# Optimization experiments

Measured on AMD Instinct MI355X. Metric: run time of the kernel, lower is better.

Reference implementation:

```python
import jax, jax.numpy as jnp
import numpy as np

B, N, C = 4, 2048, 768
H = 12
D = C // H  # 64
HID = 4 * C  # 3072
EPS = 1e-5


def layer_norm(x, g, b):
    mu = jnp.mean(x, axis=-1, keepdims=True)
    var = jnp.mean(jnp.square(x - mu), axis=-1, keepdims=True)
    return (x - mu) * jax.lax.rsqrt(var + EPS) * g + b


def setup_inputs() -> dict:
    key = jax.random.key(0)
    ks = jax.random.split(key, 12)
    s = lambda fan_in: 1.0 / np.sqrt(fan_in)
    return {
        "x": jax.random.normal(ks[0], (B, N, C), jnp.float32),
        "ln1_g": jnp.ones((C,), jnp.float32),
        "ln1_b": jnp.zeros((C,), jnp.float32),
        "qkv_w": jax.random.normal(ks[1], (3 * C, C), jnp.float32) * s(C),
        "proj_w": jax.random.normal(ks[2], (C, C), jnp.float32) * s(C),
        "proj_b": jnp.zeros((C,), jnp.float32),
        "ln2_g": jnp.ones((C,), jnp.float32),
        "ln2_b": jnp.zeros((C,), jnp.float32),
        "fc1_w": jax.random.normal(ks[3], (HID, C), jnp.float32) * s(C),
        "fc1_b": jnp.zeros((HID,), jnp.float32),
        "fc2_w": jax.random.normal(ks[4], (C, HID), jnp.float32) * s(HID),
        "fc2_b": jnp.zeros((C,), jnp.float32),
    }


def reference(x, ln1_g, ln1_b, qkv_w, proj_w, proj_b, ln2_g, ln2_b, fc1_w, fc1_b, fc2_w, fc2_b):
    # ---- attention branch ----
    h = layer_norm(x, ln1_g, ln1_b)
    qkv = jnp.einsum('bnc,fc->bnf', h, qkv_w)            # [B,N,3C]
    qkv = qkv.reshape(B, N, 3, H, D)
    q, k, v = jnp.moveaxis(qkv, 2, 0)                     # each [B,N,H,D]
    q = jnp.transpose(q, (0, 2, 1, 3)) * (D ** -0.5)      # [B,H,N,D]
    k = jnp.transpose(k, (0, 2, 1, 3))
    v = jnp.transpose(v, (0, 2, 1, 3))
    attn = jax.nn.softmax(jnp.einsum('bhnd,bhmd->bhnm', q, k), axis=-1)
    o = jnp.einsum('bhnm,bhmd->bhnd', attn, v)            # [B,H,N,D]
    o = jnp.transpose(o, (0, 2, 1, 3)).reshape(B, N, C)
    o = jnp.einsum('bnc,oc->bno', o, proj_w) + proj_b
    x = x + o
    # ---- MLP branch ----
    h = layer_norm(x, ln2_g, ln2_b)
    h = jnp.einsum('bnc,hc->bnh', h, fc1_w) + fc1_b
    h = jax.nn.gelu(h, approximate=False)
    h = jnp.einsum('bnh,ch->bnc', h, fc2_w) + fc2_b
    return x + h
```

## Files before the change

kernel.cpp:

```cpp
#include <hip/hip_runtime.h>
#include <math.h>

typedef __bf16 bf16;
typedef __bf16 bf16x4 __attribute__((ext_vector_type(4)));
typedef __bf16 bf16x8 __attribute__((ext_vector_type(8)));
typedef float  f32x4  __attribute__((ext_vector_type(4)));

#define B_   4
#define N_   2048
#define C_   768
#define H_   12
#define T_   8192
#define HID_ 3072

typedef const __attribute__((address_space(1))) unsigned int* as1_u32;
typedef __attribute__((address_space(3))) unsigned int* as3_u32;
__device__ __forceinline__ void gl_lds16(const void* g, void* l) {
    __builtin_amdgcn_global_load_lds((as1_u32)g, (as3_u32)l, 16, 0, 0);
}

__global__ __launch_bounds__(256)
void ln_kernel(const float* __restrict__ inp, const float* __restrict__ g,
               const float* __restrict__ bsh, bf16* __restrict__ out)
{
    int wave = threadIdx.x >> 6, lane = threadIdx.x & 63;
    long long row = (long long)blockIdx.x * 4 + wave;
    const float* p = inp + row * C_;
    float v[12];
    #pragma unroll
    for (int i = 0; i < 12; i++) v[i] = p[i * 64 + lane];
    float s = 0.f, s2 = 0.f;
    #pragma unroll
    for (int i = 0; i < 12; i++) { s += v[i]; s2 += v[i] * v[i]; }
    #pragma unroll
    for (int m = 1; m < 64; m <<= 1) {
        s  += __shfl_xor(s,  m, 64);
        s2 += __shfl_xor(s2, m, 64);
    }
    float mu  = s  * (1.f / C_);
    float var = s2 * (1.f / C_) - mu * mu;
    float rs  = rsqrtf(var + 1e-5f);
    bf16* o = out + row * C_;
    #pragma unroll
    for (int i = 0; i < 12; i++) {
        int c = i * 64 + lane;
        o[c] = (bf16)(((v[i] - mu) * rs) * g[c] + bsh[c]);
    }
}

template<int MODE>
__global__ __launch_bounds__(256)
void gemm_bt(const bf16* __restrict__ A, const float* __restrict__ Bw,
             int M, int N, int K,
             const float* __restrict__ bias,
             void* out, bf16* out2)
{
    __shared__ bf16 At[2][128 * 32];
    __shared__ bf16 Bt[2][128 * 32];
    int tid  = threadIdx.x;
    int lane = tid & 63, wave = tid >> 6;
    int quad = lane >> 4, l15 = lane & 15;
    int bm = blockIdx.x, bn = blockIdx.y;
    int wm = wave >> 1, wn = wave & 1;
    int swz = (l15 >> 1) & 3;

    f32x4 acc[4][4];
    f32x4 zero = {0.f, 0.f, 0.f, 0.f};
    #pragma unroll
    for (int mt = 0; mt < 4; mt++)
        #pragma unroll
        for (int nt = 0; nt < 4; nt++) acc[mt][nt] = zero;

    int arow = tid >> 2;
    int aq   = (tid & 3) ^ ((arow >> 1) & 3);
    const bf16*  ag0 = A  + (size_t)(bm * 128 + arow) * K + aq * 8;
    const float* bg0 = Bw + (size_t)(bn * 128 + arow) * K + aq * 8;

    gl_lds16(ag0,                    &At[0][tid * 8]);
    gl_lds16(ag0 + (size_t)64 * K,   &At[0][2048 + tid * 8]);
    {
        f32x4 b0a = *(const f32x4*)(bg0);
        f32x4 b0b = *(const f32x4*)(bg0 + 4);
        f32x4 b1a = *(const f32x4*)(bg0 + (size_t)64 * K);
        f32x4 b1b = *(const f32x4*)(bg0 + (size_t)64 * K + 4);
        bf16x8 b0, b1;
        #pragma unroll
        for (int j = 0; j < 4; j++) {
            b0[j] = (bf16)b0a[j]; b0[4 + j] = (bf16)b0b[j];
            b1[j] = (bf16)b1a[j]; b1[4 + j] = (bf16)b1b[j];
        }
        *(bf16x8*)(&Bt[0][tid * 8])        = b0;
        *(bf16x8*)(&Bt[0][2048 + tid * 8]) = b1;
    }
    __syncthreads();

    int nk = K >> 5;
    f32x4 pba, pbb, pca, pcb;
    for (int kt = 0; kt < nk; kt++) {
        int cur = kt & 1, nxt = cur ^ 1;
        if (kt + 1 < nk) {
            const bf16*  ag = ag0 + (size_t)(kt + 1) * 32;
            const float* bg = bg0 + (size_t)(kt + 1) * 32;
            gl_lds16(ag,                  &At[nxt][tid * 8]);
            gl_lds16(ag + (size_t)64 * K, &At[nxt][2048 + tid * 8]);
            pba = *(const f32x4*)(bg);
            pbb = *(const f32x4*)(bg + 4);
            pca = *(const f32x4*)(bg + (size_t)64 * K);
            pcb = *(const f32x4*)(bg + (size_t)64 * K + 4);
        }

        bf16x8 af[4], bfr[4];
        #pragma unroll
        for (int mt = 0; mt < 4; mt++)
            af[mt] = *(const bf16x8*)(&At[cur][wm * 2048 + (mt * 16 + l15) * 32 + ((quad ^ swz) << 3)]);
        #pragma unroll
        for (int nt = 0; nt < 4; nt++)
            bfr[nt] = *(const bf16x8*)(&Bt[cur][wn * 2048 + (nt * 16 + l15) * 32 + ((quad ^ swz) << 3)]);
        #pragma unroll
        for (int mt = 0; mt < 4; mt++)
            #pragma unroll
            for (int nt = 0; nt < 4; nt++)
                acc[mt][nt] = __builtin_amdgcn_mfma_f32_16x16x32_bf16(
                    af[mt], bfr[nt], acc[mt][nt], 0, 0, 0);

        if (kt + 1 < nk) {
            bf16x8 b0, b1;
            #pragma unroll
            for (int j = 0; j < 4; j++) {
                b0[j] = (bf16)pba[j]; b0[4 + j] = (bf16)pbb[j];
                b1[j] = (bf16)pca[j]; b1[4 + j] = (bf16)pcb[j];
            }
            *(bf16x8*)(&Bt[nxt][tid * 8])        = b0;
            *(bf16x8*)(&Bt[nxt][2048 + tid * 8]) = b1;
        }
        __syncthreads();
    }

    if (MODE == 3) {
        if (bn < 12) {
            #pragma unroll
            for (int nt = 0; nt < 4; nt++) {
                int col = bn * 128 + wn * 64 + nt * 16 + l15;
                #pragma unroll
                for (int mt = 0; mt < 4; mt++)
                    #pragma unroll
                    for (int r = 0; r < 4; r++) {
                        int row = bm * 128 + wm * 64 + mt * 16 + quad * 4 + r;
                        ((bf16*)out)[(size_t)row * 1536 + col] = (bf16)acc[mt][nt][r];
                    }
            }
        } else {
            int b = bm >> 4;
            #pragma unroll
            for (int nt = 0; nt < 4; nt++) {
                int vcol = bn * 128 - 1536 + wn * 64 + nt * 16 + l15;
                int h = vcol >> 6, d = vcol & 63;
                size_t rowbase = ((size_t)(b * H_ + h) * 64 + d) * N_;
                #pragma unroll
                for (int mt = 0; mt < 4; mt++) {
                    int n0 = (bm & 15) * 128 + wm * 64 + mt * 16 + quad * 4;
                    bf16x4 pv;
                    #pragma unroll
                    for (int r = 0; r < 4; r++) pv[r] = (bf16)acc[mt][nt][r];
                    *(bf16x4*)(&out2[rowbase + n0]) = pv;
                }
            }
        }
    } else {
        #pragma unroll
        for (int nt = 0; nt < 4; nt++) {
            int col = bn * 128 + wn * 64 + nt * 16 + l15;
            float bv = bias[col];
            #pragma unroll
            for (int mt = 0; mt < 4; mt++) {
                #pragma unroll
                for (int r = 0; r < 4; r++) {
                    int row = bm * 128 + wm * 64 + mt * 16 + quad * 4 + r;
                    size_t idx = (size_t)row * N + col;
                    float v = acc[mt][nt][r] + bv;
                    float ge = 0.5f * v * (1.f + erff(v * 0.70710678118f));
                    ((bf16*)out)[idx] = (bf16)ge;
                }
            }
        }
    }
}

__global__ __launch_bounds__(256)
void gemm64(const bf16* __restrict__ A, const float* __restrict__ Bw,
            int K, const float* __restrict__ bias,
            const float* resid_f, float* out)
{
    __shared__ bf16 At[2][128 * 32];
    __shared__ bf16 Bt[2][64 * 32];
    int tid  = threadIdx.x;
    int lane = tid & 63, wave = tid >> 6;
    int quad = lane >> 4, l15 = lane & 15;
    int bm = blockIdx.x, bn = blockIdx.y;
    int wm = wave >> 1, wn = wave & 1;
    int swz = (l15 >> 1) & 3;

    f32x4 acc[4][2];
    f32x4 zero = {0.f, 0.f, 0.f, 0.f};
    #pragma unroll
    for (int mt = 0; mt < 4; mt++)
        #pragma unroll
        for (int nt = 0; nt < 2; nt++) acc[mt][nt] = zero;

    int arow = tid >> 2;
    int aq   = (tid & 3) ^ ((arow >> 1) & 3);
    const bf16*  ag0 = A  + (size_t)(bm * 128 + arow) * K + aq * 8;
    const float* bg0 = Bw + (size_t)(bn * 64  + arow) * K + aq * 8;

    gl_lds16(ag0,                  &At[0][tid * 8]);
    gl_lds16(ag0 + (size_t)64 * K, &At[0][2048 + tid * 8]);
    {
        f32x4 ba = *(const f32x4*)(bg0);
        f32x4 bb = *(const f32x4*)(bg0 + 4);
        bf16x8 b0;
        #pragma unroll
        for (int j = 0; j < 4; j++) { b0[j] = (bf16)ba[j]; b0[4 + j] = (bf16)bb[j]; }
        *(bf16x8*)(&Bt[0][tid * 8]) = b0;
    }
    __syncthreads();

    int nk = K >> 5;
    f32x4 pba, pbb;
    for (int kt = 0; kt < nk; kt++) {
        int cur = kt & 1, nxt = cur ^ 1;
        if (kt + 1 < nk) {
            const bf16*  ag = ag0 + (size_t)(kt + 1) * 32;
            const float* bg = bg0 + (size_t)(kt + 1) * 32;
            gl_lds16(ag,                  &At[nxt][tid * 8]);
            gl_lds16(ag + (size_t)64 * K, &At[nxt][2048 + tid * 8]);
            pba = *(const f32x4*)(bg);
            pbb = *(const f32x4*)(bg + 4);
        }

        bf16x8 af[4], bfr[2];
        #pragma unroll
        for (int mt = 0; mt < 4; mt++)
            af[mt] = *(const bf16x8*)(&At[cur][wm * 2048 + (mt * 16 + l15) * 32 + ((quad ^ swz) << 3)]);
        #pragma unroll
        for (int nt = 0; nt < 2; nt++)
            bfr[nt] = *(const bf16x8*)(&Bt[cur][(wn * 32 + nt * 16 + l15) * 32 + ((quad ^ swz) << 3)]);
        #pragma unroll
        for (int mt = 0; mt < 4; mt++)
            #pragma unroll
            for (int nt = 0; nt < 2; nt++)
                acc[mt][nt] = __builtin_amdgcn_mfma_f32_16x16x32_bf16(
                    af[mt], bfr[nt], acc[mt][nt], 0, 0, 0);

        if (kt + 1 < nk) {
            bf16x8 b0;
            #pragma unroll
            for (int j = 0; j < 4; j++) { b0[j] = (bf16)pba[j]; b0[4 + j] = (bf16)pbb[j]; }
            *(bf16x8*)(&Bt[nxt][tid * 8]) = b0;
        }
        __syncthreads();
    }

    #pragma unroll
    for (int nt = 0; nt < 2; nt++) {
        int col = bn * 64 + wn * 32 + nt * 16 + l15;
        float bv = bias[col];
        #pragma unroll
        for (int mt = 0; mt < 4; mt++) {
            #pragma unroll
            for (int r = 0; r < 4; r++) {
                int row = bm * 128 + wm * 64 + mt * 16 + quad * 4 + r;
                size_t idx = (size_t)row * C_ + col;
                out[idx] = acc[mt][nt][r] + bv + resid_f[idx];
            }
        }
    }
}

__global__ __launch_bounds__(256)
void attn_kernel(const bf16* __restrict__ qk, const bf16* __restrict__ vt,
                 bf16* __restrict__ o)
{
    __shared__ bf16 Kt[2][64 * 64];
    __shared__ bf16 Vt[2][64 * 64];
    __shared__ bf16 Pt[4][2][16 * 64];

    int tid = threadIdx.x, lane = tid & 63, wave = tid >> 6;
    int quad = lane >> 4, l15 = lane & 15;
    int swz = (l15 & 7);
    int blk = blockIdx.x;
    int qb = blk & 15;
    int bh = blk >> 4;
    int b = bh / H_, h = bh % H_;

    const bf16* qbase = qk + (size_t)(b * N_) * 1536 + h * 64;
    const bf16* kbase = qbase + 768;
    const bf16* vtb   = vt + (size_t)(bh * 64) * N_;

    bf16x8 qf[2][2];
    #pragma unroll
    for (int qi = 0; qi < 2; qi++) {
        int q = qb * 128 + wave * 32 + qi * 16 + l15;
        const bf16* qp = qbase + (size_t)q * 1536 + quad * 8;
        qf[qi][0] = *(const bf16x8*)(qp);
        qf[qi][1] = *(const bf16x8*)(qp + 32);
    }

    int srow = tid >> 3, schk = tid & 7;
    int soA = srow * 64 + ((schk ^ (srow & 7)) << 3);
    int soB = (srow + 32) * 64 + ((schk ^ (srow & 7)) << 3);

    bf16x8 kr0, kr1, vr0, vr1;
    const bf16* kg0 = kbase + (size_t)srow * 1536 + schk * 8;
    const bf16* vg0 = vtb + (size_t)srow * N_ + schk * 8;

    {
        kr0 = *(const bf16x8*)(kg0);
        kr1 = *(const bf16x8*)(kg0 + (size_t)32 * 1536);
        vr0 = *(const bf16x8*)(vg0);
        vr1 = *(const bf16x8*)(vg0 + (size_t)32 * N_);
        *(bf16x8*)(&Kt[0][soA]) = kr0;  *(bf16x8*)(&Kt[0][soB]) = kr1;
        *(bf16x8*)(&Vt[0][soA]) = vr0;  *(bf16x8*)(&Vt[0][soB]) = vr1;
    }
    __syncthreads();

    f32x4 oacc[2][4];
    f32x4 zero = {0.f, 0.f, 0.f, 0.f};
    #pragma unroll
    for (int qi = 0; qi < 2; qi++)
        #pragma unroll
        for (int nt = 0; nt < 4; nt++) oacc[qi][nt] = zero;
    float mrun[2] = {-1e30f, -1e30f}, lrun[2] = {0.f, 0.f};

    for (int kt = 0; kt < 32; kt++) {
        int cur = kt & 1;
        if (kt < 31) {
            const bf16* kg = kg0 + (size_t)(kt + 1) * 64 * 1536;
            const bf16* vg = vg0 + (size_t)(kt + 1) * 64;
            kr0 = *(const bf16x8*)(kg);
            kr1 = *(const bf16x8*)(kg + (size_t)32 * 1536);
            vr0 = *(const bf16x8*)(vg);
            vr1 = *(const bf16x8*)(vg + (size_t)32 * N_);
        }
        const bf16* KtC = &Kt[cur][0];
        const bf16* VtC = &Vt[cur][0];

        #pragma unroll
        for (int qi = 0; qi < 2; qi++) {
            f32x4 s[4];
            #pragma unroll
            for (int nt = 0; nt < 4; nt++) {
                const bf16* krow = KtC + (nt * 16 + l15) * 64;
                bf16x8 ka0 = *(const bf16x8*)(krow + ((quad ^ swz) << 3));
                bf16x8 ka1 = *(const bf16x8*)(krow + (((4 + quad) ^ swz) << 3));
                f32x4 sv = zero;
                sv = __builtin_amdgcn_mfma_f32_16x16x32_bf16(ka0, qf[qi][0], sv, 0, 0, 0);
                sv = __builtin_amdgcn_mfma_f32_16x16x32_bf16(ka1, qf[qi][1], sv, 0, 0, 0);
                s[nt] = sv;
            }
            float mx = -1e30f;
            #pragma unroll
            for (int nt = 0; nt < 4; nt++)
                #pragma unroll
                for (int r = 0; r < 4; r++) mx = fmaxf(mx, s[nt][r]);
            mx = fmaxf(mx, __shfl_xor(mx, 16, 64));
            mx = fmaxf(mx, __shfl_xor(mx, 32, 64));
            float mnew = fmaxf(mrun[qi], mx * 0.125f);
            float al   = __expf(mrun[qi] - mnew);
            mrun[qi] = mnew;
            float ps = 0.f;
            #pragma unroll
            for (int nt = 0; nt < 4; nt++)
                #pragma unroll
                for (int r = 0; r < 4; r++) {
                    float pv = __expf(s[nt][r] * 0.125f - mnew);
                    s[nt][r] = pv;
                    ps += pv;
                }
            ps += __shfl_xor(ps, 16, 64);
            ps += __shfl_xor(ps, 32, 64);
            lrun[qi] = lrun[qi] * al + ps;
            #pragma unroll
            for (int nt = 0; nt < 4; nt++) oacc[qi][nt] *= al;
            bf16* pw = &Pt[wave][qi][0];
            #pragma unroll
            for (int nt = 0; nt < 4; nt++) {
                bf16x4 pk;
                #pragma unroll
                for (int r = 0; r < 4; r++) pk[r] = (bf16)s[nt][r];
                int ofs = l15 * 64 + (((nt * 2 + (quad >> 1)) ^ swz) << 3) + ((quad & 1) << 2);
                *(bf16x4*)(&pw[ofs]) = pk;
            }
        }

        #pragma unroll
        for (int kc = 0; kc < 2; kc++) {
            int pofs = l15 * 64 + (((kc * 4 + quad) ^ swz) << 3);
            bf16x8 pb0 = *(const bf16x8*)(&Pt[wave][0][pofs]);
            bf16x8 pb1 = *(const bf16x8*)(&Pt[wave][1][pofs]);
            #pragma unroll
            for (int nt = 0; nt < 4; nt++) {
                bf16x8 va = *(const bf16x8*)(VtC + (nt * 16 + l15) * 64 +
                                             (((kc * 4 + quad) ^ swz) << 3));
                oacc[0][nt] = __builtin_amdgcn_mfma_f32_16x16x32_bf16(va, pb0, oacc[0][nt], 0, 0, 0);
                oacc[1][nt] = __builtin_amdgcn_mfma_f32_16x16x32_bf16(va, pb1, oacc[1][nt], 0, 0, 0);
            }
        }

        if (kt < 31) {
            int nxt = cur ^ 1;
            *(bf16x8*)(&Kt[nxt][soA]) = kr0;  *(bf16x8*)(&Kt[nxt][soB]) = kr1;
            *(bf16x8*)(&Vt[nxt][soA]) = vr0;  *(bf16x8*)(&Vt[nxt][soB]) = vr1;
        }
        __syncthreads();
    }

    #pragma unroll
    for (int qi = 0; qi < 2; qi++) {
        int q = qb * 128 + wave * 32 + qi * 16 + l15;
        float inv = 1.f / lrun[qi];
        bf16* ob = o + (size_t)(b * N_ + q) * C_ + h * 64 + quad * 4;
        #pragma unroll
        for (int nt = 0; nt < 4; nt++) {
            bf16x4 pk;
            #pragma unroll
            for (int r = 0; r < 4; r++) pk[r] = (bf16)(oacc[qi][nt][r] * inv);
            *(bf16x4*)(&ob[nt * 16]) = pk;
        }
    }
}

extern "C" void kernel_launch(void* const* d_in, const int* in_sizes, int n_in,
                              void* d_out, int out_size, void* d_ws, size_t ws_size,
                              hipStream_t stream)
{
    const float* x      = (const float*)d_in[0];
    const float* ln1_g  = (const float*)d_in[1];
    const float* ln1_b  = (const float*)d_in[2];
    const float* qkv_w  = (const float*)d_in[3];
    const float* proj_w = (const float*)d_in[4];
    const float* proj_b = (const float*)d_in[5];
    const float* ln2_g  = (const float*)d_in[6];
    const float* ln2_b  = (const float*)d_in[7];
    const float* fc1_w  = (const float*)d_in[8];
    const float* fc1_b  = (const float*)d_in[9];
    const float* fc2_w  = (const float*)d_in[10];
    const float* fc2_b  = (const float*)d_in[11];
    float* out = (float*)d_out;

    char* ws = (char*)d_ws;
    bf16* QK = (bf16*)ws;
    bf16* VT = (bf16*)(ws + (size_t)T_ * 1536 * 2);
    bf16* G  = (bf16*)ws;
    bf16* R1 = (bf16*)(ws + (size_t)T_ * HID_ * 2);

    ln_kernel<<<T_ / 4, 256, 0, stream>>>(x, ln1_g, ln1_b, R1);
    gemm_bt<3><<<dim3(T_ / 128, 2304 / 128), 256, 0, stream>>>(
        R1, qkv_w, T_, 2304, C_, nullptr, QK, VT);
    attn_kernel<<<48 * 16, 256, 0, stream>>>(QK, VT, R1);
    gemm64<<<dim3(T_ / 128, C_ / 64), 256, 0, stream>>>(
        R1, proj_w, C_, proj_b, x, out);
    ln_kernel<<<T_ / 4, 256, 0, stream>>>(out, ln2_g, ln2_b, R1);
    gemm_bt<2><<<dim3(T_ / 128, HID_ / 128), 256, 0, stream>>>(
        R1, fc1_w, T_, HID_, C_, fc1_b, G, nullptr);
    gemm64<<<dim3(T_ / 128, C_ / 64), 256, 0, stream>>>(
        G, fc2_w, HID_, fc2_b, out, out);
}
```

Before: 495.6 us.

## Retile residual GEMMs to 64x256, use exp2 softmax and fast GELU

```diff
diff --git a/kernel.cpp b/kernel.cpp
--- a/kernel.cpp
+++ b/kernel.cpp
@@ -12,6 +12,17 @@
 #define H_   12
 #define T_   8192
 #define HID_ 3072
+
+#if __has_builtin(__builtin_amdgcn_exp2f)
+#define EXP2F __builtin_amdgcn_exp2f
+#else
+#define EXP2F exp2f
+#endif
+#if __has_builtin(__builtin_amdgcn_rcpf)
+#define RCPF __builtin_amdgcn_rcpf
+#else
+#define RCPF(x) (1.0f / (x))
+#endif
 
 typedef const __attribute__((address_space(1))) unsigned int* as1_u32;
 typedef __attribute__((address_space(3))) unsigned int* as3_u32;
@@ -178,7 +189,10 @@
                     int row = bm * 128 + wm * 64 + mt * 16 + quad * 4 + r;
                     size_t idx = (size_t)row * N + col;
                     float v = acc[mt][nt][r] + bv;
-                    float ge = 0.5f * v * (1.f + erff(v * 0.70710678118f));
+                    float t = v * v;
+                    float u = v * fmaf(t, 0.0356774081f, 0.7978845608f);
+                    float e = EXP2F(u * 2.8853900818f);
+                    float ge = v - v * RCPF(e + 1.f);
                     ((bf16*)out)[idx] = (bf16)ge;
                 }
             }
@@ -187,12 +201,12 @@
 }
 
 __global__ __launch_bounds__(256)
-void gemm64(const bf16* __restrict__ A, const float* __restrict__ Bw,
-            int K, const float* __restrict__ bias,
-            const float* resid_f, float* out)
+void gemm_n256(const bf16* __restrict__ A, const float* __restrict__ Bw,
+               int K, const float* __restrict__ bias,
+               const float* resid_f, float* out)
 {
-    __shared__ bf16 At[2][128 * 32];
-    __shared__ bf16 Bt[2][64 * 32];
+    __shared__ bf16 At[2][64 * 32];
+    __shared__ bf16 Bt[2][256 * 32];
     int tid  = threadIdx.x;
     int lane = tid & 63, wave = tid >> 6;
     int quad = lane >> 4, l15 = lane & 15;
@@ -200,75 +214,84 @@
     int wm = wave >> 1, wn = wave & 1;
     int swz = (l15 >> 1) & 3;
 
-    f32x4 acc[4][2];
+    f32x4 acc[2][8];
     f32x4 zero = {0.f, 0.f, 0.f, 0.f};
     #pragma unroll
-    for (int mt = 0; mt < 4; mt++)
-        #pragma unroll
-        for (int nt = 0; nt < 2; nt++) acc[mt][nt] = zero;
+    for (int mt = 0; mt < 2; mt++)
+        #pragma unroll
+        for (int nt = 0; nt < 8; nt++) acc[mt][nt] = zero;
 
     int arow = tid >> 2;
     int aq   = (tid & 3) ^ ((arow >> 1) & 3);
-    const bf16*  ag0 = A  + (size_t)(bm * 128 + arow) * K + aq * 8;
-    const float* bg0 = Bw + (size_t)(bn * 64  + arow) * K + aq * 8;
-
-    gl_lds16(ag0,                  &At[0][tid * 8]);
-    gl_lds16(ag0 + (size_t)64 * K, &At[0][2048 + tid * 8]);
+    const bf16*  ag0 = A  + (size_t)(bm * 64 + arow) * K + aq * 8;
+    int bperm = (tid >> 1) & 3;
+    const float* bg0 = Bw + (size_t)(bn * 256 + tid) * K;
+
+    gl_lds16(ag0, &At[0][tid * 8]);
     {
-        f32x4 ba = *(const f32x4*)(bg0);
-        f32x4 bb = *(const f32x4*)(bg0 + 4);
-        bf16x8 b0;
-        #pragma unroll
-        for (int j = 0; j < 4; j++) { b0[j] = (bf16)ba[j]; b0[4 + j] = (bf16)bb[j]; }
-        *(bf16x8*)(&Bt[0][tid * 8]) = b0;
+        #pragma unroll
+        for (int c = 0; c < 4; c++) {
+            f32x4 xa = *(const f32x4*)(bg0 + c * 8);
+            f32x4 xb = *(const f32x4*)(bg0 + c * 8 + 4);
+            bf16x8 b;
+            #pragma unroll
+            for (int j = 0; j < 4; j++) { b[j] = (bf16)xa[j]; b[4 + j] = (bf16)xb[j]; }
+            *(bf16x8*)(&Bt[0][tid * 32 + ((c ^ bperm) << 3)]) = b;
+        }
     }
     __syncthreads();
 
     int nk = K >> 5;
-    f32x4 pba, pbb;
+    f32x4 pb[8];
     for (int kt = 0; kt < nk; kt++) {
         int cur = kt & 1, nxt = cur ^ 1;
         if (kt + 1 < nk) {
-            const bf16*  ag = ag0 + (size_t)(kt + 1) * 32;
+            gl_lds16(ag0 + (size_t)(kt + 1) * 32, &At[nxt][tid * 8]);
             const float* bg = bg0 + (size_t)(kt + 1) * 32;
-            gl_lds16(ag,                  &At[nxt][tid * 8]);
-            gl_lds16(ag + (size_t)64 * K, &At[nxt][2048 + tid * 8]);
-            pba = *(const f32x4*)(bg);
-            pbb = *(const f32x4*)(bg + 4);
-        }
-
-        bf16x8 af[4], bfr[2];
-        #pragma unroll
-        for (int mt = 0; mt < 4; mt++)
-            af[mt] = *(const bf16x8*)(&At[cur][wm * 2048 + (mt * 16 + l15) * 32 + ((quad ^ swz) << 3)]);
-        #pragma unroll
-        for (int nt = 0; nt < 2; nt++)
-            bfr[nt] = *(const bf16x8*)(&Bt[cur][(wn * 32 + nt * 16 + l15) * 32 + ((quad ^ swz) << 3)]);
-        #pragma unroll
-        for (int mt = 0; mt < 4; mt++)
-            #pragma unroll
-            for (int nt = 0; nt < 2; nt++)
+            #pragma unroll
+            for (int c = 0; c < 4; c++) {
+                pb[2 * c]     = *(const f32x4*)(bg + c * 8);
+                pb[2 * c + 1] = *(const f32x4*)(bg + c * 8 + 4);
+            }
+        }
+
+        bf16x8 af[2], bfr[8];
+        #pragma unroll
+        for (int mt = 0; mt < 2; mt++)
+            af[mt] = *(const bf16x8*)(&At[cur][(wm * 32 + mt * 16 + l15) * 32 + ((quad ^ swz) << 3)]);
+        #pragma unroll
+        for (int nt = 0; nt < 8; nt++)
+            bfr[nt] = *(const bf16x8*)(&Bt[cur][(wn * 128 + nt * 16 + l15) * 32 + ((quad ^ swz) << 3)]);
+        #pragma unroll
+        for (int mt = 0; mt < 2; mt++)
+            #pragma unroll
+            for (int nt = 0; nt < 8; nt++)
                 acc[mt][nt] = __builtin_amdgcn_mfma_f32_16x16x32_bf16(
                     af[mt], bfr[nt], acc[mt][nt], 0, 0, 0);
 
         if (kt + 1 < nk) {
-            bf16x8 b0;
-            #pragma unroll
-            for (int j = 0; j < 4; j++) { b0[j] = (bf16)pba[j]; b0[4 + j] = (bf16)pbb[j]; }
-            *(bf16x8*)(&Bt[nxt][tid * 8]) = b0;
+            #pragma unroll
+            for (int c = 0; c < 4; c++) {
+                bf16x8 b;
+                #pragma unroll
+                for (int j = 0; j < 4; j++) {
+                    b[j] = (bf16)pb[2 * c][j]; b[4 + j] = (bf16)pb[2 * c + 1][j];
+                }
+                *(bf16x8*)(&Bt[nxt][tid * 32 + ((c ^ bperm) << 3)]) = b;
+            }
         }
         __syncthreads();
     }
 
     #pragma unroll
-    for (int nt = 0; nt < 2; nt++) {
-        int col = bn * 64 + wn * 32 + nt * 16 + l15;
+    for (int nt = 0; nt < 8; nt++) {
+        int col = bn * 256 + wn * 128 + nt * 16 + l15;
         float bv = bias[col];
         #pragma unroll
-        for (int mt = 0; mt < 4; mt++) {
+        for (int mt = 0; mt < 2; mt++) {
             #pragma unroll
             for (int r = 0; r < 4; r++) {
-                int row = bm * 128 + wm * 64 + mt * 16 + quad * 4 + r;
+                int row = bm * 64 + wm * 32 + mt * 16 + quad * 4 + r;
                 size_t idx = (size_t)row * C_ + col;
                 out[idx] = acc[mt][nt][r] + bv + resid_f[idx];
             }
@@ -283,6 +306,8 @@
     __shared__ bf16 Kt[2][64 * 64];
     __shared__ bf16 Vt[2][64 * 64];
     __shared__ bf16 Pt[4][2][16 * 64];
+
+    const float SC = 0.18033688011112042f;
 
     int tid = threadIdx.x, lane = tid & 63, wave = tid >> 6;
     int quad = lane >> 4, l15 = lane & 15;
@@ -344,49 +369,58 @@
         const bf16* KtC = &Kt[cur][0];
         const bf16* VtC = &Vt[cur][0];
 
+        f32x4 s[2][4];
+        #pragma unroll
+        for (int nt = 0; nt < 4; nt++) {
+            const bf16* krow = KtC + (nt * 16 + l15) * 64;
+            bf16x8 ka0 = *(const bf16x8*)(krow + ((quad ^ swz) << 3));
+            bf16x8 ka1 = *(const bf16x8*)(krow + (((4 + quad) ^ swz) << 3));
+            f32x4 sv0 = zero, sv1 = zero;
+            sv0 = __builtin_amdgcn_mfma_f32_16x16x32_bf16(ka0, qf[0][0], sv0, 0, 0, 0);
+            sv0 = __builtin_amdgcn_mfma_f32_16x16x32_bf16(ka1, qf[0][1], sv0, 0, 0, 0);
+            sv1 = __builtin_amdgcn_mfma_f32_16x16x32_bf16(ka0, qf[1][0], sv1, 0, 0, 0);
+            sv1 = __builtin_amdgcn_mfma_f32_16x16x32_bf16(ka1, qf[1][1], sv1, 0, 0, 0);
+            s[0][nt] = sv0;
+            s[1][nt] = sv1;
+        }
+
         #pragma unroll
         for (int qi = 0; qi < 2; qi++) {
-            f32x4 s[4];
-            #pragma unroll
-            for (int nt = 0; nt < 4; nt++) {
-                const bf16* krow = KtC + (nt * 16 + l15) * 64;
-                bf16x8 ka0 = *(const bf16x8*)(krow + ((quad ^ swz) << 3));
-                bf16x8 ka1 = *(const bf16x8*)(krow + (((4 + quad) ^ swz) << 3));
-                f32x4 sv = zero;
-                sv = __builtin_amdgcn_mfma_f32_16x16x32_bf16(ka0, qf[qi][0], sv, 0, 0, 0);
-                sv = __builtin_amdgcn_mfma_f32_16x16x32_bf16(ka1, qf[qi][1], sv, 0, 0, 0);
-                s[nt] = sv;
-            }
             float mx = -1e30f;
             #pragma unroll
             for (int nt = 0; nt < 4; nt++)
                 #pragma unroll
-                for (int r = 0; r < 4; r++) mx = fmaxf(mx, s[nt][r]);
+                for (int r = 0; r < 4; r++) mx = fmaxf(mx, s[qi][nt][r]);
             mx = fmaxf(mx, __shfl_xor(mx, 16, 64));
             mx = fmaxf(mx, __shfl_xor(mx, 32, 64));
-            float mnew = fmaxf(mrun[qi], mx * 0.125f);
-            float al   = __expf(mrun[qi] - mnew);
-            mrun[qi] = mnew;
+            float m2 = mx * SC;
+            if (__any(m2 > mrun[qi])) {
+                float mnew = fmaxf(mrun[qi], m2);
+                float al = EXP2F(mrun[qi] - mnew);
+                mrun[qi] = mnew;
+                lrun[qi] *= al;
+                #pragma unroll
+                for (int nt = 0; nt < 4; nt++) oacc[qi][nt] *= al;
+            }
+            float mcur = mrun[qi];
             float ps = 0.f;
             #pragma unroll
             for (int nt = 0; nt < 4; nt++)
                 #pragma unroll
                 for (int r = 0; r < 4; r++) {
-                    float pv = __expf(s[nt][r] * 0.125f - mnew);
-                    s[nt][r] = pv;
+                    float pv = EXP2F(fmaf(s[qi][nt][r], SC, -mcur));
+                    s[qi][nt][r] = pv;
                     ps += pv;
                 }
             ps += __shfl_xor(ps, 16, 64);
             ps += __shfl_xor(ps, 32, 64);
-            lrun[qi] = lrun[qi] * al + ps;
-            #pragma unroll
-            for (int nt = 0; nt < 4; nt++) oacc[qi][nt] *= al;
+            lrun[qi] += ps;
             bf16* pw = &Pt[wave][qi][0];
             #pragma unroll
             for (int nt = 0; nt < 4; nt++) {
                 bf16x4 pk;
                 #pragma unroll
-                for (int r = 0; r < 4; r++) pk[r] = (bf16)s[nt][r];
+                for (int r = 0; r < 4; r++) pk[r] = (bf16)s[qi][nt][r];
                 int ofs = l15 * 64 + (((nt * 2 + (quad >> 1)) ^ swz) << 3) + ((quad & 1) << 2);
                 *(bf16x4*)(&pw[ofs]) = pk;
             }
@@ -457,11 +491,11 @@
     gemm_bt<3><<<dim3(T_ / 128, 2304 / 128), 256, 0, stream>>>(
         R1, qkv_w, T_, 2304, C_, nullptr, QK, VT);
     attn_kernel<<<48 * 16, 256, 0, stream>>>(QK, VT, R1);
-    gemm64<<<dim3(T_ / 128, C_ / 64), 256, 0, stream>>>(
+    gemm_n256<<<dim3(T_ / 64, C_ / 256), 256, 0, stream>>>(
         R1, proj_w, C_, proj_b, x, out);
     ln_kernel<<<T_ / 4, 256, 0, stream>>>(out, ln2_g, ln2_b, R1);
     gemm_bt<2><<<dim3(T_ / 128, HID_ / 128), 256, 0, stream>>>(
         R1, fc1_w, T_, HID_, C_, fc1_b, G, nullptr);
-    gemm64<<<dim3(T_ / 128, C_ / 64), 256, 0, stream>>>(
+    gemm_n256<<<dim3(T_ / 64, C_ / 256), 256, 0, stream>>>(
         G, fc2_w, HID_, fc2_b, out, out);
 }
```

After: 618.8 us. +24.9%, slower.
